# Kernel tuning notes

Hardware: AMD Instinct MI355X
Metric: run time of the kernel (lower is better)

The kernel has to match this reference:

```python
import jax, jax.numpy as jnp
import numpy as np

B, ISIZE, HSIZE = 256, 256, 512
CLIPVAL = 2.0

def _linear(x, W, b):
    # torch nn.Linear: y = x @ W.T + b, W is [out, in]
    return x @ W.T + b

def setup_inputs() -> dict:
    key = jax.random.key(0)
    ks = jax.random.split(key, 24)
    d = {}
    d['inputs'] = jax.random.normal(ks[0], (B, ISIZE), jnp.float32)
    d['h0'] = jax.random.normal(ks[1], (B, HSIZE), jnp.float32) * 0.1
    d['c0'] = jax.random.normal(ks[2], (B, HSIZE), jnp.float32) * 0.1
    d['hebb'] = jax.random.normal(ks[3], (B, HSIZE, HSIZE), jnp.float32) * 0.01
    d['w'] = 0.02 * jax.random.uniform(ks[4], (HSIZE, HSIZE), jnp.float32) - 0.01
    d['alpha'] = 0.0001 * jax.random.uniform(ks[5], (1, 1, HSIZE), jnp.float32)
    scale_h = 1.0 / np.sqrt(HSIZE)
    scale_i = 1.0 / np.sqrt(ISIZE)
    d['h2f_w'] = jax.random.uniform(ks[6], (HSIZE, HSIZE), jnp.float32, -scale_h, scale_h)
    d['h2f_b'] = jax.random.uniform(ks[7], (HSIZE,), jnp.float32, -scale_h, scale_h)
    d['h2i_w'] = jax.random.uniform(ks[8], (HSIZE, HSIZE), jnp.float32, -scale_h, scale_h)
    d['h2i_b'] = jax.random.uniform(ks[9], (HSIZE,), jnp.float32, -scale_h, scale_h)
    d['h2opt_w'] = jax.random.uniform(ks[10], (HSIZE, HSIZE), jnp.float32, -scale_h, scale_h)
    d['h2opt_b'] = jax.random.uniform(ks[11], (HSIZE,), jnp.float32, -scale_h, scale_h)
    d['x2f_w'] = jax.random.uniform(ks[12], (HSIZE, ISIZE), jnp.float32, -scale_i, scale_i)
    d['x2f_b'] = jax.random.uniform(ks[13], (HSIZE,), jnp.float32, -scale_i, scale_i)
    d['x2i_w'] = jax.random.uniform(ks[14], (HSIZE, ISIZE), jnp.float32, -scale_i, scale_i)
    d['x2i_b'] = jax.random.uniform(ks[15], (HSIZE,), jnp.float32, -scale_i, scale_i)
    d['x2opt_w'] = jax.random.uniform(ks[16], (HSIZE, ISIZE), jnp.float32, -scale_i, scale_i)
    d['x2opt_b'] = jax.random.uniform(ks[17], (HSIZE,), jnp.float32, -scale_i, scale_i)
    d['x2c_w'] = jax.random.uniform(ks[18], (HSIZE, ISIZE), jnp.float32, -scale_i, scale_i)
    d['x2c_b'] = jax.random.uniform(ks[19], (HSIZE,), jnp.float32, -scale_i, scale_i)
    d['h2mod_w'] = jax.random.uniform(ks[20], (1, HSIZE), jnp.float32, -scale_h, scale_h)
    d['h2mod_b'] = jax.random.uniform(ks[21], (1,), jnp.float32, -scale_h, scale_h)
    d['modfanout_w'] = jax.random.uniform(ks[22], (HSIZE, 1), jnp.float32, -1.0, 1.0)
    d['modfanout_b'] = jax.random.uniform(ks[23], (HSIZE,), jnp.float32, -1.0, 1.0)
    return d

def reference(inputs, h0, c0, hebb, w, alpha,
              h2f_w, h2f_b, h2i_w, h2i_b, h2opt_w, h2opt_b,
              x2f_w, x2f_b, x2i_w, x2i_b, x2opt_w, x2opt_b, x2c_w, x2c_b,
              h2mod_w, h2mod_b, modfanout_w, modfanout_b):
    # gates
    fgt = jax.nn.sigmoid(_linear(inputs, x2f_w, x2f_b) + _linear(h0, h2f_w, h2f_b))
    ipt = jax.nn.sigmoid(_linear(inputs, x2i_w, x2i_b) + _linear(h0, h2i_w, h2i_b))
    opt = jax.nn.sigmoid(_linear(inputs, x2opt_w, x2opt_b) + _linear(h0, h2opt_w, h2opt_b))
    # plastic recurrent matmul: h [B,h] x (w + alpha*hebb) [B,h,h]
    M = w[None, :, :] + alpha * hebb  # [B, h, h]
    h2coutput = jnp.einsum('bh,bhk->bk', h0, M)
    inputstocell = jnp.tanh(_linear(inputs, x2c_w, x2c_b) + h2coutput)
    cell = fgt * c0 + ipt * inputstocell
    hactiv = opt * jnp.tanh(cell)
    # Hebbian outer product (hebboutput='i2c')
    deltahebb = h0[:, :, None] * inputstocell[:, None, :]  # [B, h, h]
    # modulation: modultype='modplasth2mod', modulout='fanout'
    m = jnp.tanh(_linear(hactiv, h2mod_w, h2mod_b))  # [B, 1]
    fan = m[:, 0][:, None] * modfanout_w[:, 0][None, :] + modfanout_b[None, :]  # [B, h]
    myeta = fan[:, None, :]  # [B, 1, h]
    # cliptype='clip'
    hebb_new = jnp.clip(hebb + myeta * deltahebb, -CLIPVAL, CLIPVAL)
    return hactiv, cell, hebb_new
```

## Files before the change

### kernel.cpp

```cpp
#include <hip/hip_runtime.h>
#include <math.h>

#define BATCH 256
#define ISZ 256
#define H 512
#define BH (BATCH * H)
#define CLIPV 2.0f

__device__ __forceinline__ float sigmoidf_(float x) { return 1.0f / (1.0f + expf(-x)); }

#define BT 64
#define KT 32
#define LDSP (BT + 4)

__global__ __launch_bounds__(256) void small_gemms(
    const float* __restrict__ x, const float* __restrict__ h0,
    const float* __restrict__ x2f_w, const float* __restrict__ x2f_b,
    const float* __restrict__ h2f_w, const float* __restrict__ h2f_b,
    const float* __restrict__ x2i_w, const float* __restrict__ x2i_b,
    const float* __restrict__ h2i_w, const float* __restrict__ h2i_b,
    const float* __restrict__ x2o_w, const float* __restrict__ x2o_b,
    const float* __restrict__ h2o_w, const float* __restrict__ h2o_b,
    const float* __restrict__ x2c_w, const float* __restrict__ x2c_b,
    const float* __restrict__ w,
    float* __restrict__ pre)
{
  __shared__ __align__(16) float As[KT][LDSP];
  __shared__ __align__(16) float Bs[KT][LDSP];
  const int z  = blockIdx.z;
  const int n0 = blockIdx.x * BT;
  const int m0 = blockIdx.y * BT;
  const int t  = threadIdx.x;
  const int tx = t & 15, ty = t >> 4;

  float acc[4][4] = {{0.0f}};

  const float* Aseg[2]; const float* Bseg[2];
  int ldaS[2], KS[2]; int nseg; bool kmajor = true;
  const float* xb = nullptr; const float* hbias = nullptr;

  if (z < 3) {
    const float* xw; const float* hw_;
    if (z == 0)      { xw = x2f_w; xb = x2f_b; hw_ = h2f_w; hbias = h2f_b; }
    else if (z == 1) { xw = x2i_w; xb = x2i_b; hw_ = h2i_w; hbias = h2i_b; }
    else             { xw = x2o_w; xb = x2o_b; hw_ = h2o_w; hbias = h2o_b; }
    Aseg[0] = x;  ldaS[0] = ISZ; Bseg[0] = xw;  KS[0] = ISZ;
    Aseg[1] = h0; ldaS[1] = H;   Bseg[1] = hw_; KS[1] = H;
    nseg = 2;
  } else if (z == 3) {
    Aseg[0] = x; ldaS[0] = ISZ; Bseg[0] = x2c_w; KS[0] = ISZ; xb = x2c_b;
    nseg = 1;
  } else {
    Aseg[0] = h0; ldaS[0] = H; Bseg[0] = w; KS[0] = H;
    nseg = 1; kmajor = false;
  }

  for (int s = 0; s < nseg; ++s) {
    const float* A  = Aseg[s];
    const float* Bm = Bseg[s];
    const int lda = ldaS[s];
    const int K   = KS[s];
    for (int kk0 = 0; kk0 < K; kk0 += KT) {
      #pragma unroll
      for (int i = 0; i < 8; ++i) {
        int l = i * 256 + t;
        int j = l & 31, r = l >> 5;
        As[j][r] = A[(size_t)(m0 + r) * lda + kk0 + j];
      }
      if (kmajor) {
        #pragma unroll
        for (int i = 0; i < 8; ++i) {
          int l = i * 256 + t;
          int j = l & 31, n = l >> 5;
          Bs[j][n] = Bm[(size_t)(n0 + n) * K + kk0 + j];
        }
      } else {
        #pragma unroll
        for (int i = 0; i < 8; ++i) {
          int l = i * 256 + t;
          int n = l & 63, j = l >> 6;
          Bs[j][n] = Bm[(size_t)(kk0 + j) * H + n0 + n];
        }
      }
      __syncthreads();
      #pragma unroll
      for (int j = 0; j < KT; ++j) {
        float4 a  = *(const float4*)&As[j][ty * 4];
        float4 bv = *(const float4*)&Bs[j][tx * 4];
        float av[4] = {a.x, a.y, a.z, a.w};
        float bw[4] = {bv.x, bv.y, bv.z, bv.w};
        #pragma unroll
        for (int r = 0; r < 4; ++r)
          #pragma unroll
          for (int c = 0; c < 4; ++c)
            acc[r][c] += av[r] * bw[c];
      }
      __syncthreads();
    }
  }

  float bias[4];
  #pragma unroll
  for (int c = 0; c < 4; ++c) {
    int n = n0 + tx * 4 + c;
    float bv = 0.0f;
    if (z < 3)       bv = xb[n] + hbias[n];
    else if (z == 3) bv = xb[n];
    bias[c] = bv;
  }
  float* outc = pre + (size_t)z * BH;
  #pragma unroll
  for (int r = 0; r < 4; ++r) {
    int m = m0 + ty * 4 + r;
    float4 o;
    o.x = acc[r][0] + bias[0];
    o.y = acc[r][1] + bias[1];
    o.z = acc[r][2] + bias[2];
    o.w = acc[r][3] + bias[3];
    *(float4*)&outc[(size_t)m * H + n0 + tx * 4] = o;
  }
}

__global__ __launch_bounds__(128) void einsum_partial(
    const float* __restrict__ h0, const float* __restrict__ hebb,
    float* __restrict__ hbpart)
{
  const int b    = blockIdx.x;
  const int hseg = blockIdx.y;
  const int t    = threadIdx.x;
  __shared__ float h0s[64];
  if (t < 64) h0s[t] = h0[b * H + hseg * 64 + t];
  __syncthreads();

  const float4* hb4 = (const float4*)(hebb + ((size_t)b * H + (size_t)hseg * 64) * H);
  float4 acc = {0.f, 0.f, 0.f, 0.f};
  #pragma unroll 8
  for (int h = 0; h < 64; ++h) {
    float4 v = hb4[(size_t)h * 128 + t];
    float s = h0s[h];
    acc.x += s * v.x; acc.y += s * v.y; acc.z += s * v.z; acc.w += s * v.w;
  }
  ((float4*)(hbpart + ((size_t)(b * 8 + hseg)) * H))[t] = acc;
}

__global__ __launch_bounds__(256) void fuse_gates(
    const float* __restrict__ pre, const float* __restrict__ hbpart,
    const float* __restrict__ c0, const float* __restrict__ alpha,
    float* __restrict__ out, float* __restrict__ itc)
{
  const int idx = blockIdx.x * 256 + threadIdx.x;
  const int k = idx & (H - 1);
  const int b = idx >> 9;
  float hb = 0.0f;
  #pragma unroll
  for (int s = 0; s < 8; ++s) hb += hbpart[((size_t)(b * 8 + s)) * H + k];
  float h2c  = pre[(size_t)4 * BH + idx] + alpha[k] * hb;
  float itcv = tanhf(pre[(size_t)3 * BH + idx] + h2c);
  float f = sigmoidf_(pre[(size_t)0 * BH + idx]);
  float i = sigmoidf_(pre[(size_t)1 * BH + idx]);
  float o = sigmoidf_(pre[(size_t)2 * BH + idx]);
  float cell = f * c0[idx] + i * itcv;
  float ha = o * tanhf(cell);
  out[idx] = ha;
  out[BH + idx] = cell;
  itc[idx] = itcv;
}

__global__ __launch_bounds__(256) void mod_eta(
    const float* __restrict__ hactiv,
    const float* __restrict__ h2mod_w, const float* __restrict__ h2mod_b,
    const float* __restrict__ mfo_w, const float* __restrict__ mfo_b,
    const float* __restrict__ itc, float* __restrict__ eta)
{
  const int b = blockIdx.x, t = threadIdx.x;
  float s = hactiv[b * H + t] * h2mod_w[t] + hactiv[b * H + 256 + t] * h2mod_w[256 + t];
  #pragma unroll
  for (int off = 32; off > 0; off >>= 1) s += __shfl_down(s, off, 64);
  __shared__ float red[4];
  __shared__ float mm;
  if ((t & 63) == 0) red[t >> 6] = s;
  __syncthreads();
  if (t == 0) mm = tanhf(red[0] + red[1] + red[2] + red[3] + h2mod_b[0]);
  __syncthreads();
  float m = mm;
  #pragma unroll
  for (int kk = t; kk < H; kk += 256) {
    float fan = m * mfo_w[kk] + mfo_b[kk];
    eta[b * H + kk] = fan * itc[b * H + kk];
  }
}

__global__ __launch_bounds__(256) void hebb_update(
    const float* __restrict__ hebb, const float* __restrict__ h0,
    const float* __restrict__ eta, float* __restrict__ out)
{
  const size_t g = (size_t)blockIdx.x * 256 + threadIdx.x;
  float4 v = ((const float4*)hebb)[g];
  const int k4  = (int)(g & 127);
  const int row = (int)(g >> 7);
  const int b   = row >> 9;
  float4 e = ((const float4*)eta)[(b << 7) + k4];
  float s = h0[row];
  float4 r;
  r.x = fminf(fmaxf(v.x + s * e.x, -CLIPV), CLIPV);
  r.y = fminf(fmaxf(v.y + s * e.y, -CLIPV), CLIPV);
  r.z = fminf(fmaxf(v.z + s * e.z, -CLIPV), CLIPV);
  r.w = fminf(fmaxf(v.w + s * e.w, -CLIPV), CLIPV);
  ((float4*)out)[(size_t)(2 * BH / 4) + g] = r;
}

extern "C" void kernel_launch(void* const* d_in, const int* in_sizes, int n_in,
                              void* d_out, int out_size, void* d_ws, size_t ws_size,
                              hipStream_t stream) {
  const float* x       = (const float*)d_in[0];
  const float* h0      = (const float*)d_in[1];
  const float* c0      = (const float*)d_in[2];
  const float* hebb    = (const float*)d_in[3];
  const float* w       = (const float*)d_in[4];
  const float* alpha   = (const float*)d_in[5];
  const float* h2f_w   = (const float*)d_in[6];
  const float* h2f_b   = (const float*)d_in[7];
  const float* h2i_w   = (const float*)d_in[8];
  const float* h2i_b   = (const float*)d_in[9];
  const float* h2o_w   = (const float*)d_in[10];
  const float* h2o_b   = (const float*)d_in[11];
  const float* x2f_w   = (const float*)d_in[12];
  const float* x2f_b   = (const float*)d_in[13];
  const float* x2i_w   = (const float*)d_in[14];
  const float* x2i_b   = (const float*)d_in[15];
  const float* x2o_w   = (const float*)d_in[16];
  const float* x2o_b   = (const float*)d_in[17];
  const float* x2c_w   = (const float*)d_in[18];
  const float* x2c_b   = (const float*)d_in[19];
  const float* h2mod_w = (const float*)d_in[20];
  const float* h2mod_b = (const float*)d_in[21];
  const float* mfo_w   = (const float*)d_in[22];
  const float* mfo_b   = (const float*)d_in[23];

  float* out = (float*)d_out;
  float* ws  = (float*)d_ws;

  float* pre    = ws;
  float* hbpart = pre + (size_t)5 * BH;
  float* itc    = hbpart + (size_t)BATCH * 8 * H;
  float* eta    = itc + BH;

  small_gemms<<<dim3(8, 4, 5), 256, 0, stream>>>(
      x, h0, x2f_w, x2f_b, h2f_w, h2f_b, x2i_w, x2i_b, h2i_w, h2i_b,
      x2o_w, x2o_b, h2o_w, h2o_b, x2c_w, x2c_b, w, pre);

  einsum_partial<<<dim3(BATCH, 8), 128, 0, stream>>>(h0, hebb, hbpart);

  fuse_gates<<<BH / 256, 256, 0, stream>>>(pre, hbpart, c0, alpha, out, itc);

  mod_eta<<<BATCH, 256, 0, stream>>>(out, h2mod_w, h2mod_b, mfo_w, mfo_b, itc, eta);

  hebb_update<<<(BH * H / 4) / 256, 256, 0, stream>>>(hebb, h0, eta, out);
}
```

Baseline: 675.9 us.

## Fuse plastic einsum, gates, modulation and hebb update into one register-resident kernel

Replaces four kernels (einsum partials, gate fusion, modulation eta, hebb update) with a single kernel per batch row of 1024 threads. Each thread keeps its 64 float4 slices of the batch's hebb matrix in registers, so hebb is read from HBM once instead of twice, and the partial-sum, itc and eta workspace buffers go away. The cost is very high register pressure (256 floats per thread), which can spill to scratch or cap occupancy to one block per CU. Only 256 blocks are launched, which limits latency hiding.

```diff
diff --git a/kernel.cpp b/kernel.cpp
--- a/kernel.cpp
+++ b/kernel.cpp
@@ -121,92 +121,101 @@
   }
 }
 
-__global__ __launch_bounds__(128) void einsum_partial(
-    const float* __restrict__ h0, const float* __restrict__ hebb,
-    float* __restrict__ hbpart)
-{
-  const int b    = blockIdx.x;
-  const int hseg = blockIdx.y;
-  const int t    = threadIdx.x;
-  __shared__ float h0s[64];
-  if (t < 64) h0s[t] = h0[b * H + hseg * 64 + t];
-  __syncthreads();
-
-  const float4* hb4 = (const float4*)(hebb + ((size_t)b * H + (size_t)hseg * 64) * H);
-  float4 acc = {0.f, 0.f, 0.f, 0.f};
-  #pragma unroll 8
-  for (int h = 0; h < 64; ++h) {
-    float4 v = hb4[(size_t)h * 128 + t];
-    float s = h0s[h];
-    acc.x += s * v.x; acc.y += s * v.y; acc.z += s * v.z; acc.w += s * v.w;
-  }
-  ((float4*)(hbpart + ((size_t)(b * 8 + hseg)) * H))[t] = acc;
-}
-
-__global__ __launch_bounds__(256) void fuse_gates(
-    const float* __restrict__ pre, const float* __restrict__ hbpart,
+__global__ __launch_bounds__(1024, 4) void fused_plastic(
+    const float* __restrict__ hebb, const float* __restrict__ h0,
     const float* __restrict__ c0, const float* __restrict__ alpha,
-    float* __restrict__ out, float* __restrict__ itc)
-{
-  const int idx = blockIdx.x * 256 + threadIdx.x;
-  const int k = idx & (H - 1);
-  const int b = idx >> 9;
-  float hb = 0.0f;
-  #pragma unroll
-  for (int s = 0; s < 8; ++s) hb += hbpart[((size_t)(b * 8 + s)) * H + k];
-  float h2c  = pre[(size_t)4 * BH + idx] + alpha[k] * hb;
-  float itcv = tanhf(pre[(size_t)3 * BH + idx] + h2c);
-  float f = sigmoidf_(pre[(size_t)0 * BH + idx]);
-  float i = sigmoidf_(pre[(size_t)1 * BH + idx]);
-  float o = sigmoidf_(pre[(size_t)2 * BH + idx]);
-  float cell = f * c0[idx] + i * itcv;
-  float ha = o * tanhf(cell);
-  out[idx] = ha;
-  out[BH + idx] = cell;
-  itc[idx] = itcv;
-}
-
-__global__ __launch_bounds__(256) void mod_eta(
-    const float* __restrict__ hactiv,
+    const float* __restrict__ pre,
     const float* __restrict__ h2mod_w, const float* __restrict__ h2mod_b,
     const float* __restrict__ mfo_w, const float* __restrict__ mfo_b,
-    const float* __restrict__ itc, float* __restrict__ eta)
+    float* __restrict__ out)
 {
-  const int b = blockIdx.x, t = threadIdx.x;
-  float s = hactiv[b * H + t] * h2mod_w[t] + hactiv[b * H + 256 + t] * h2mod_w[256 + t];
-  #pragma unroll
-  for (int off = 32; off > 0; off >>= 1) s += __shfl_down(s, off, 64);
-  __shared__ float red[4];
-  __shared__ float mm;
-  if ((t & 63) == 0) red[t >> 6] = s;
-  __syncthreads();
-  if (t == 0) mm = tanhf(red[0] + red[1] + red[2] + red[3] + h2mod_b[0]);
-  __syncthreads();
-  float m = mm;
-  #pragma unroll
-  for (int kk = t; kk < H; kk += 256) {
-    float fan = m * mfo_w[kk] + mfo_b[kk];
-    eta[b * H + kk] = fan * itc[b * H + kk];
-  }
-}
-
-__global__ __launch_bounds__(256) void hebb_update(
-    const float* __restrict__ hebb, const float* __restrict__ h0,
-    const float* __restrict__ eta, float* __restrict__ out)
-{
-  const size_t g = (size_t)blockIdx.x * 256 + threadIdx.x;
-  float4 v = ((const float4*)hebb)[g];
-  const int k4  = (int)(g & 127);
-  const int row = (int)(g >> 7);
-  const int b   = row >> 9;
-  float4 e = ((const float4*)eta)[(b << 7) + k4];
-  float s = h0[row];
-  float4 r;
-  r.x = fminf(fmaxf(v.x + s * e.x, -CLIPV), CLIPV);
-  r.y = fminf(fmaxf(v.y + s * e.y, -CLIPV), CLIPV);
-  r.z = fminf(fmaxf(v.z + s * e.z, -CLIPV), CLIPV);
-  r.w = fminf(fmaxf(v.w + s * e.w, -CLIPV), CLIPV);
-  ((float4*)out)[(size_t)(2 * BH / 4) + g] = r;
+  const int b  = blockIdx.x;
+  const int t  = threadIdx.x;
+  const int g  = t >> 7;
+  const int k4 = t & 127;
+
+  __shared__ float  h0s[H];
+  __shared__ float4 hbp[8][128];
+  __shared__ float4 hbs4[128];
+  __shared__ float  itcs[H];
+  __shared__ float4 eta4s[128];
+  __shared__ float  wred[16];
+  __shared__ float  mm;
+
+  if (t < H) h0s[t] = h0[b * H + t];
+  __syncthreads();
+
+  const float4* hb4 = (const float4*)(hebb + (size_t)b * H * H);
+  float4 st[64];
+  float4 ps = {0.f, 0.f, 0.f, 0.f};
+  #pragma unroll
+  for (int i = 0; i < 64; ++i) {
+    st[i] = hb4[i * 1024 + t];
+    float s = h0s[i * 8 + g];
+    ps.x += s * st[i].x; ps.y += s * st[i].y;
+    ps.z += s * st[i].z; ps.w += s * st[i].w;
+  }
+  hbp[g][k4] = ps;
+  __syncthreads();
+
+  if (t < 128) {
+    float4 a = hbp[0][t];
+    #pragma unroll
+    for (int q = 1; q < 8; ++q) {
+      float4 v = hbp[q][t];
+      a.x += v.x; a.y += v.y; a.z += v.z; a.w += v.w;
+    }
+    hbs4[t] = a;
+  }
+  __syncthreads();
+
+  float s_red = 0.0f;
+  if (t < H) {
+    const int idx = b * H + t;
+    float hbv  = ((const float*)hbs4)[t];
+    float h2c  = pre[(size_t)4 * BH + idx] + alpha[t] * hbv;
+    float itcv = tanhf(pre[(size_t)3 * BH + idx] + h2c);
+    float f = sigmoidf_(pre[(size_t)0 * BH + idx]);
+    float i = sigmoidf_(pre[(size_t)1 * BH + idx]);
+    float o = sigmoidf_(pre[(size_t)2 * BH + idx]);
+    float cell = f * c0[idx] + i * itcv;
+    float ha   = o * tanhf(cell);
+    out[idx]      = ha;
+    out[BH + idx] = cell;
+    itcs[t] = itcv;
+    s_red = ha * h2mod_w[t];
+  }
+
+  #pragma unroll
+  for (int off = 32; off > 0; off >>= 1) s_red += __shfl_down(s_red, off, 64);
+  if ((t & 63) == 0) wred[t >> 6] = s_red;
+  __syncthreads();
+  if (t == 0) {
+    float a = 0.0f;
+    #pragma unroll
+    for (int q = 0; q < 16; ++q) a += wred[q];
+    mm = tanhf(a + h2mod_b[0]);
+  }
+  __syncthreads();
+
+  if (t < H) {
+    float fan = mm * mfo_w[t] + mfo_b[t];
+    ((float*)eta4s)[t] = fan * itcs[t];
+  }
+  __syncthreads();
+
+  float4 e = eta4s[k4];
+  float4* outp = (float4*)(out + (size_t)2 * BH) + (size_t)b * (H * H / 4);
+  #pragma unroll
+  for (int i = 0; i < 64; ++i) {
+    float s = h0s[i * 8 + g];
+    float4 r;
+    r.x = fminf(fmaxf(st[i].x + s * e.x, -CLIPV), CLIPV);
+    r.y = fminf(fmaxf(st[i].y + s * e.y, -CLIPV), CLIPV);
+    r.z = fminf(fmaxf(st[i].z + s * e.z, -CLIPV), CLIPV);
+    r.w = fminf(fmaxf(st[i].w + s * e.w, -CLIPV), CLIPV);
+    outp[i * 1024 + t] = r;
+  }
 }
 
 extern "C" void kernel_launch(void* const* d_in, const int* in_sizes, int n_in,
@@ -240,20 +249,12 @@
   float* out = (float*)d_out;
   float* ws  = (float*)d_ws;
 
-  float* pre    = ws;
-  float* hbpart = pre + (size_t)5 * BH;
-  float* itc    = hbpart + (size_t)BATCH * 8 * H;
-  float* eta    = itc + BH;
+  float* pre = ws;
 
   small_gemms<<<dim3(8, 4, 5), 256, 0, stream>>>(
       x, h0, x2f_w, x2f_b, h2f_w, h2f_b, x2i_w, x2i_b, h2i_w, h2i_b,
       x2o_w, x2o_b, h2o_w, h2o_b, x2c_w, x2c_b, w, pre);
 
-  einsum_partial<<<dim3(BATCH, 8), 128, 0, stream>>>(h0, hebb, hbpart);
-
-  fuse_gates<<<BH / 256, 256, 0, stream>>>(pre, hbpart, c0, alpha, out, itc);
-
-  mod_eta<<<BATCH, 256, 0, stream>>>(out, h2mod_w, h2mod_b, mfo_w, mfo_b, itc, eta);
-
-  hebb_update<<<(BH * H / 4) / 256, 256, 0, stream>>>(hebb, h0, eta, out);
+  fused_plastic<<<BATCH, 1024, 0, stream>>>(
+      hebb, h0, c0, alpha, pre, h2mod_w, h2mod_b, mfo_w, mfo_b, out);
 }
```

Result: slower. 727.8 us (+7.7%).
